# Performance work log

Measured on AMD Instinct MI355X. Metric: run time of the kernel, lower is better.

The kernel has to match this reference:

```python
import jax, jax.numpy as jnp
import numpy as np

N_HEAD = 8

def _l2norm(x, eps=1e-12):
    # F.normalize(p=2, dim=-1): x / max(||x||_2, eps)
    return x / jnp.maximum(jnp.linalg.norm(x, axis=-1, keepdims=True), eps)

def setup_inputs() -> dict:
    key = jax.random.key(0)
    ks = jax.random.split(key, 9)
    B, L, E = 2, 2048, 512
    s = 0.02
    return {
        "query": jax.random.normal(ks[0], (B, L, E), dtype=jnp.float32),
        "Wq": s * jax.random.normal(ks[1], (E, E), dtype=jnp.float32),
        "bq": jnp.zeros((E,), dtype=jnp.float32),
        "Wk": s * jax.random.normal(ks[2], (E, E), dtype=jnp.float32),
        "bk": jnp.zeros((E,), dtype=jnp.float32),
        "Wv": s * jax.random.normal(ks[3], (E, E), dtype=jnp.float32),
        "bv": jnp.zeros((E,), dtype=jnp.float32),
        "Wo": s * jax.random.normal(ks[4], (E, E), dtype=jnp.float32),
        "bo": jnp.zeros((E,), dtype=jnp.float32),
    }

def reference(query, Wq, bq, Wk, bk, Wv, bv, Wo, bo):
    B, L, E = query.shape
    H = N_HEAD
    hd = E // H
    # Faithful to torch: .view(tgt_len, bsz, E) is a RESHAPE, not a transpose.
    x = query.reshape(L, B, E)
    q = jax.nn.relu(x @ Wq.T + bq)
    k = jax.nn.relu(x @ Wk.T + bk)
    v = x @ Wv.T + bv
    q = _l2norm(q)
    k = _l2norm(k)
    # (L, B, E) -> (L, B*H, hd) -> (B*H, L, hd)
    q_ = q.reshape(L, B * H, hd).transpose(1, 0, 2)
    k_ = k.reshape(L, B * H, hd).transpose(1, 0, 2)
    v_ = v.reshape(L, B * H, hd).transpose(1, 0, 2)
    # Causal linear attention: cumulative outer-product of k,v then contract with q.
    kv = jnp.einsum('nld,nlm->nldm', k_, v_)      # [B*H, L, hd, hd]
    kv_cum = jnp.cumsum(kv, axis=1)
    out = jnp.einsum('nld,nldm->nlm', q_, kv_cum)  # [B*H, L, hd]
    out = out.transpose(1, 0, 2).reshape(L, B, E)
    out = out @ Wo.T + bo
    return out.reshape(B, L, E)
```

## Files before the change

kernel.cpp:

```cpp
#include <hip/hip_runtime.h>
#include <hip/hip_bf16.h>

typedef __attribute__((ext_vector_type(8))) short short8;
typedef __attribute__((ext_vector_type(4))) float f32x4;
using bf16 = __hip_bfloat16;

__device__ __forceinline__ unsigned short f2bf(float f) {
    unsigned u = __float_as_uint(f);
    u += 0x7fff + ((u >> 16) & 1);
    return (unsigned short)(u >> 16);
}
__device__ __forceinline__ float bf2f(unsigned short s) {
    return __uint_as_float(((unsigned)s) << 16);
}
__device__ __forceinline__ void gl_lds16(const unsigned short* g, unsigned short* l) {
    __builtin_amdgcn_global_load_lds(
        (const __attribute__((address_space(1))) unsigned int*)g,
        (__attribute__((address_space(3))) unsigned int*)l, 16, 0, 0);
}


__global__ __launch_bounds__(256) void pack_kernel(
    const float* __restrict__ X, const float* __restrict__ Wq, const float* __restrict__ Wk,
    const float* __restrict__ Wv, const float* __restrict__ Wo,
    bf16* __restrict__ Xp, bf16* __restrict__ Wqp, bf16* __restrict__ Wkp,
    bf16* __restrict__ Wvp, bf16* __restrict__ Wop, float* __restrict__ ssq)
{
    __shared__ __align__(16) unsigned short sm[4096];
    int id = blockIdx.x;
    int tid = threadIdx.x;
    if (id < 8) {
        int zi = id * 1024 + tid * 4;
        *(float4*)&ssq[zi] = make_float4(0.f, 0.f, 0.f, 0.f);
    }
    const float* src; unsigned short* dst; int g, sc;
    if (id < 512) { src = X; dst = (unsigned short*)Xp; g = id >> 3; sc = id & 7; }
    else {
        int t = id - 512; int wsel = t >> 6; int u = t & 63;
        g = u >> 3; sc = u & 7;
        src = (wsel == 0) ? Wq : ((wsel == 1) ? Wk : ((wsel == 2) ? Wv : Wo));
        dst = (unsigned short*)((wsel == 0) ? Wqp : ((wsel == 1) ? Wkp : ((wsel == 2) ? Wvp : Wop)));
    }
    int r = tid >> 2, kq = tid & 3;
    const float* sp = src + (size_t)(g * 64 + r) * 512 + sc * 64 + kq * 16;
    #pragma unroll
    for (int i = 0; i < 4; ++i) {
        float4 v = *(const float4*)(sp + i * 4);
        int kk = kq * 16 + i * 4;
        int sl = kk >> 3, el = kk & 7;
        ushort4 u4;
        u4.x = f2bf(v.x); u4.y = f2bf(v.y); u4.z = f2bf(v.z); u4.w = f2bf(v.w);
        *(ushort4*)&sm[(sl * 64 + r) * 8 + el] = u4;
    }
    __syncthreads();
    unsigned short* dp = dst + (size_t)g * 32768 + sc * 4096;
    *(uint4*)(dp + tid * 16)     = *(const uint4*)&sm[tid * 16];
    *(uint4*)(dp + tid * 16 + 8) = *(const uint4*)&sm[tid * 16 + 8];
}

__global__ __launch_bounds__(256) void qkv_gemm_kernel(
    const bf16* __restrict__ Xp,
    const bf16* __restrict__ W0p, const bf16* __restrict__ W1p, const bf16* __restrict__ W2p,
    const float* __restrict__ b0, const float* __restrict__ b1, const float* __restrict__ b2,
    bf16* __restrict__ O0, bf16* __restrict__ O1, bf16* __restrict__ O2,
    float* __restrict__ ssq)
{
    __shared__ __align__(16) unsigned short smem[8192];
    unsigned short* As = smem;
    unsigned short* Bs = smem + 2048;
    int z = blockIdx.z;
    const unsigned short* Wg = (const unsigned short*)((z == 0) ? W0p : ((z == 1) ? W1p : W2p));
    const float* bias = (z == 0) ? b0 : ((z == 1) ? b1 : b2);
    unsigned short* Out = (unsigned short*)((z == 0) ? O0 : ((z == 1) ? O1 : O2));
    const unsigned short* Ag = (const unsigned short*)Xp;

    int g  = blockIdx.x;
    int gB = blockIdx.y * 2;
    int m0 = g * 64;
    int n0 = blockIdx.y * 128;
    int tid = threadIdx.x;
    int lane = tid & 63;
    int w = tid >> 6;
    int wm = (w >> 1) * 32;
    int wn = (w & 1) * 64;
    int fr = lane & 15, qf = lane >> 4;

    f32x4 zero4 = {0.f, 0.f, 0.f, 0.f};
    f32x4 acc[2][4];
    #pragma unroll
    for (int t = 0; t < 2; ++t)
        #pragma unroll
        for (int u = 0; u < 4; ++u) acc[t][u] = zero4;

    for (int kw = 0; kw < 16; ++kw) {
        int s0 = kw * 4;
        __syncthreads();
        gl_lds16(Ag + ((size_t)(g * 64 + s0 + w) * 64 + lane) * 8, As + w * 512);
        gl_lds16(Wg + ((size_t)(gB * 64 + s0 + w) * 64 + lane) * 8, Bs + w * 1024);
        gl_lds16(Wg + ((size_t)((gB + 1) * 64 + s0 + w) * 64 + lane) * 8, Bs + w * 1024 + 512);
        __syncthreads();
        short8 af[2], bfr[4];
        #pragma unroll
        for (int t = 0; t < 2; ++t) af[t] = *(const short8*)&As[(qf * 64 + wm + t * 16 + fr) * 8];
        #pragma unroll
        for (int u = 0; u < 4; ++u) bfr[u] = *(const short8*)&Bs[(qf * 128 + wn + u * 16 + fr) * 8];
        #pragma unroll
        for (int t = 0; t < 2; ++t)
            #pragma unroll
            for (int u = 0; u < 4; ++u)
                acc[t][u] = __builtin_amdgcn_mfma_f32_16x16x32_bf16(af[t], bfr[u], acc[t][u], 0, 0, 0);
    }

    bool relu = (z < 2);
    int rb = qf * 4;
    #pragma unroll
    for (int t = 0; t < 2; ++t)
        #pragma unroll
        for (int u = 0; u < 4; ++u) {
            float bv = bias[n0 + wn + u * 16 + fr];
            #pragma unroll
            for (int r = 0; r < 4; ++r) {
                float v = acc[t][u][r] + bv;
                if (relu) v = fmaxf(v, 0.f);
                acc[t][u][r] = v;
            }
        }
    if (relu) {
        #pragma unroll
        for (int t = 0; t < 2; ++t)
            #pragma unroll
            for (int r = 0; r < 4; ++r) {
                float s = 0.f;
                #pragma unroll
                for (int u = 0; u < 4; ++u) s += acc[t][u][r] * acc[t][u][r];
                #pragma unroll
                for (int off = 1; off < 16; off <<= 1) s += __shfl_xor(s, off, 64);
                if (fr == 0) atomicAdd(&ssq[z * 4096 + m0 + wm + t * 16 + rb + r], s);
            }
    }
    __syncthreads();
    #pragma unroll
    for (int t = 0; t < 2; ++t)
        #pragma unroll
        for (int u = 0; u < 4; ++u)
            #pragma unroll
            for (int r = 0; r < 4; ++r)
                smem[(wm + t * 16 + rb + r) * 128 + wn + u * 16 + fr] = f2bf(acc[t][u][r]);
    __syncthreads();
    #pragma unroll
    for (int rep = 0; rep < 4; ++rep) {
        int idx8 = rep * 256 + tid;
        int row = idx8 >> 4, col8 = (idx8 & 15) * 8;
        *(uint4*)(Out + (size_t)(m0 + row) * 512 + n0 + col8) = *(const uint4*)&smem[row * 128 + col8];
    }
}

__global__ __launch_bounds__(256) void chunk_kv_kernel(
    const bf16* __restrict__ Kb, const bf16* __restrict__ Vb,
    const float* __restrict__ ssq, float* __restrict__ ScT, bf16* __restrict__ Vt_g)
{
    int n = blockIdx.x >> 5, c = blockIdx.x & 31;
    int b = n >> 3, h = n & 7;
    __shared__ float Ks[64 * 64];
    __shared__ float Vs[64 * 64];
    const unsigned short* Kg = (const unsigned short*)Kb;
    const unsigned short* Vg = (const unsigned short*)Vb;
    int tid = threadIdx.x;
    int td = tid >> 4, tm = tid & 15;
    int d0 = td * 4, m0 = tm * 4;
    #pragma unroll
    for (int rep = 0; rep < 4; ++rep) {
        int idx = rep * 1024 + tid * 4;
        int j = idx >> 6, d = idx & 63;
        int grow = (c * 64 + j) * 2 + b;
        ushort4 ku = *(const ushort4*)&Kg[(size_t)grow * 512 + h * 64 + d];
        ushort4 vu = *(const ushort4*)&Vg[(size_t)grow * 512 + h * 64 + d];
        float rk = 1.f / fmaxf(sqrtf(ssq[4096 + grow]), 1e-12f);
        *(float4*)&Ks[j * 64 + d] = make_float4(bf2f(ku.x), bf2f(ku.y), bf2f(ku.z), bf2f(ku.w));
        *(float4*)&Vs[j * 64 + d] = make_float4(bf2f(vu.x) * rk, bf2f(vu.y) * rk,
                                                bf2f(vu.z) * rk, bf2f(vu.w) * rk);
    }
    __syncthreads();
    float acc[4][4] = {};
    for (int j = 0; j < 64; ++j) {
        float4 kv = *(const float4*)&Ks[j * 64 + d0];
        float4 vv = *(const float4*)&Vs[j * 64 + m0];
        acc[0][0] += kv.x*vv.x; acc[0][1] += kv.x*vv.y; acc[0][2] += kv.x*vv.z; acc[0][3] += kv.x*vv.w;
        acc[1][0] += kv.y*vv.x; acc[1][1] += kv.y*vv.y; acc[1][2] += kv.y*vv.z; acc[1][3] += kv.y*vv.w;
        acc[2][0] += kv.z*vv.x; acc[2][1] += kv.z*vv.y; acc[2][2] += kv.z*vv.z; acc[2][3] += kv.z*vv.w;
        acc[3][0] += kv.w*vv.x; acc[3][1] += kv.w*vv.y; acc[3][2] += kv.w*vv.z; acc[3][3] += kv.w*vv.w;
    }
    int vm = tid & 63, vj0 = (tid >> 6) * 16;
    unsigned short tmp[16];
    #pragma unroll
    for (int i = 0; i < 16; ++i) tmp[i] = f2bf(Vs[(vj0 + i) * 64 + vm]);
    size_t vtoff = (size_t)n * 131072 + (size_t)vm * 2048 + c * 64 + vj0;
    *(uint4*)((unsigned short*)Vt_g + vtoff)     = *(uint4*)&tmp[0];
    *(uint4*)((unsigned short*)Vt_g + vtoff + 8) = *(uint4*)&tmp[8];

    float* outp = ScT + (size_t)blockIdx.x * 4096;
    #pragma unroll
    for (int j2 = 0; j2 < 4; ++j2) {
        float4 o4 = make_float4(acc[0][j2], acc[1][j2], acc[2][j2], acc[3][j2]);
        *(float4*)&outp[(m0 + j2) * 64 + d0] = o4;
    }
}

__global__ __launch_bounds__(256) void prefix_kernel(const float* __restrict__ ScT, bf16* __restrict__ SpT)
{
    int n = blockIdx.x >> 4;
    int idx = ((blockIdx.x & 15) << 8) + threadIdx.x;
    size_t base = (size_t)n * 131072 + idx;
    unsigned short* sp = (unsigned short*)SpT;
    float run = 0.f;
    #pragma unroll
    for (int c = 0; c < 32; ++c) {
        size_t off = base + (size_t)c * 4096;
        sp[off] = f2bf(run);
        run += ScT[off];
    }
}

__global__ __launch_bounds__(256) void attn_kernel(
    const bf16* __restrict__ Qb, const bf16* __restrict__ Kb,
    const bf16* __restrict__ Vt_g, const bf16* __restrict__ SpT_g,
    const float* __restrict__ ssq, bf16* __restrict__ AOb)
{
    int n = blockIdx.x >> 5, c = blockIdx.x & 31;
    int b = n >> 3, h = n & 7;
    __shared__ unsigned short Qs[64 * 72];
    __shared__ unsigned short Ks[64 * 72];
    __shared__ unsigned short Vt[64 * 72];
    __shared__ unsigned short Ps[4 * 16 * 40];
    int tid = threadIdx.x;
    int lane = tid & 63;
    int w = tid >> 6;
    int fr = lane & 15, q = lane >> 4;

    const unsigned short* Qg = (const unsigned short*)Qb;
    const unsigned short* Kg = (const unsigned short*)Kb;
    const unsigned short* Vg = (const unsigned short*)Vt_g;

    #pragma unroll
    for (int rep = 0; rep < 2; ++rep) {
        int idx = rep * 256 + tid;
        int l = idx >> 3, dc = (idx & 7) * 8;
        size_t goff = (size_t)((c * 64 + l) * 2 + b) * 512 + h * 64 + dc;
        *(uint4*)&Qs[l * 72 + dc] = *(const uint4*)(Qg + goff);
        *(uint4*)&Ks[l * 72 + dc] = *(const uint4*)(Kg + goff);
        int m = l, jc = dc;
        *(uint4*)&Vt[m * 72 + jc] =
            *(const uint4*)(Vg + (size_t)n * 131072 + (size_t)m * 2048 + c * 64 + jc);
    }
    __syncthreads();

    short8 qf[2];
    #pragma unroll
    for (int kh = 0; kh < 2; ++kh)
        qf[kh] = *(const short8*)&Qs[(w * 16 + fr) * 72 + kh * 32 + q * 8];

    f32x4 zero4 = {0.f, 0.f, 0.f, 0.f};
    f32x4 oacc[4];
    #pragma unroll
    for (int mt = 0; mt < 4; ++mt) oacc[mt] = zero4;

    const unsigned short* spg = (const unsigned short*)SpT_g + (size_t)blockIdx.x * 4096;
    #pragma unroll
    for (int mt = 0; mt < 4; ++mt) {
        #pragma unroll
        for (int kh = 0; kh < 2; ++kh) {
            short8 sf = *(const short8*)&spg[(mt * 16 + fr) * 64 + kh * 32 + q * 8];
            oacc[mt] = __builtin_amdgcn_mfma_f32_16x16x32_bf16(qf[kh], sf, oacc[mt], 0, 0, 0);
        }
    }

    unsigned short* myPs = &Ps[w * 640];
    int rbase = q * 4;
    int njt = (w >> 1) + 1;
    for (int jt = 0; jt < njt; ++jt) {
        f32x4 pacc[2];
        pacc[0] = zero4; pacc[1] = zero4;
        #pragma unroll
        for (int jt16 = 0; jt16 < 2; ++jt16) {
            #pragma unroll
            for (int kh = 0; kh < 2; ++kh) {
                short8 kf = *(const short8*)&Ks[(jt * 32 + jt16 * 16 + fr) * 72 + kh * 32 + q * 8];
                pacc[jt16] = __builtin_amdgcn_mfma_f32_16x16x32_bf16(qf[kh], kf, pacc[jt16], 0, 0, 0);
            }
        }
        bool diag = (jt == njt - 1);
        int lloc = w * 16 + rbase;
        #pragma unroll
        for (int jt16 = 0; jt16 < 2; ++jt16)
            #pragma unroll
            for (int r = 0; r < 4; ++r) {
                int jl = jt * 32 + jt16 * 16 + fr;
                float pv = pacc[jt16][r];
                if (diag && jl > lloc + r) pv = 0.f;
                myPs[(rbase + r) * 40 + jt16 * 16 + fr] = f2bf(pv);
            }
        short8 pf = *(const short8*)&myPs[fr * 40 + q * 8];
        #pragma unroll
        for (int mt = 0; mt < 4; ++mt) {
            short8 vf = *(const short8*)&Vt[(mt * 16 + fr) * 72 + jt * 32 + q * 8];
            oacc[mt] = __builtin_amdgcn_mfma_f32_16x16x32_bf16(pf, vf, oacc[mt], 0, 0, 0);
        }
    }

    float rqv[4];
    #pragma unroll
    for (int r = 0; r < 4; ++r) {
        int flat = (c * 64 + w * 16 + rbase + r) * 2 + b;
        rqv[r] = 1.f / fmaxf(sqrtf(ssq[flat]), 1e-12f);
    }
    __syncthreads();
    #pragma unroll
    for (int mt = 0; mt < 4; ++mt)
        #pragma unroll
        for (int r = 0; r < 4; ++r)
            Qs[(w * 16 + rbase + r) * 64 + mt * 16 + fr] = f2bf(oacc[mt][r] * rqv[r]);
    __syncthreads();
    #pragma unroll
    for (int rep = 0; rep < 2; ++rep) {
        int idx8 = rep * 256 + tid;
        int l = idx8 >> 3, m8 = (idx8 & 7) * 8;
        *(uint4*)((unsigned short*)AOb + (size_t)((c * 64 + l) * 2 + b) * 512 + h * 64 + m8) =
            *(const uint4*)&Qs[l * 64 + m8];
    }
}

__global__ __launch_bounds__(256) void oproj_kernel(
    const bf16* __restrict__ A, const bf16* __restrict__ Wop,
    const float* __restrict__ bias, float* __restrict__ Out)
{
    __shared__ __align__(16) unsigned short smem[8192];
    unsigned short* As = smem;
    unsigned short* Bs = smem + 2560;
    const unsigned short* Ag = (const unsigned short*)A;
    const unsigned short* Wg = (const unsigned short*)Wop;
    int m0 = blockIdx.x * 64;
    int gy = blockIdx.y;
    int n0 = gy * 64;
    int tid = threadIdx.x;
    int lane = tid & 63;
    int w = tid >> 6;
    int fr = lane & 15, qf = lane >> 4;
    int wm = (w >> 1) * 32;
    int wn = (w & 1) * 32;
    int srow = tid >> 2;
    int skk  = (tid & 3) * 8;

    f32x4 zero4 = {0.f, 0.f, 0.f, 0.f};
    f32x4 acc[2][2];
    acc[0][0] = zero4; acc[0][1] = zero4; acc[1][0] = zero4; acc[1][1] = zero4;

    for (int kw = 0; kw < 16; ++kw) {
        int k0 = kw * 32, s0 = kw * 4;
        __syncthreads();
        *(uint4*)&As[srow * 40 + skk] = *(const uint4*)(Ag + (size_t)(m0 + srow) * 512 + k0 + skk);
        gl_lds16(Wg + ((size_t)(gy * 64 + s0 + w) * 64 + lane) * 8, Bs + w * 512);
        __syncthreads();
        short8 af[2], bf[2];
        #pragma unroll
        for (int t = 0; t < 2; ++t) af[t] = *(const short8*)&As[(wm + t * 16 + fr) * 40 + qf * 8];
        #pragma unroll
        for (int u = 0; u < 2; ++u) bf[u] = *(const short8*)&Bs[(qf * 64 + wn + u * 16 + fr) * 8];
        #pragma unroll
        for (int t = 0; t < 2; ++t)
            #pragma unroll
            for (int u = 0; u < 2; ++u)
                acc[t][u] = __builtin_amdgcn_mfma_f32_16x16x32_bf16(af[t], bf[u], acc[t][u], 0, 0, 0);
    }

    int rb = qf * 4;
    float* Cf = (float*)smem;
    __syncthreads();
    #pragma unroll
    for (int t = 0; t < 2; ++t)
        #pragma unroll
        for (int u = 0; u < 2; ++u) {
            float bv = bias[n0 + wn + u * 16 + fr];
            #pragma unroll
            for (int r = 0; r < 4; ++r)
                Cf[(wm + t * 16 + rb + r) * 64 + wn + u * 16 + fr] = acc[t][u][r] + bv;
        }
    __syncthreads();
    #pragma unroll
    for (int rep = 0; rep < 4; ++rep) {
        int idx = rep * 256 + tid;
        int row = idx >> 4, c4 = (idx & 15) * 4;
        *(float4*)(Out + (size_t)(m0 + row) * 512 + n0 + c4) = *(const float4*)&Cf[row * 64 + c4];
    }
}

extern "C" void kernel_launch(void* const* d_in, const int* in_sizes, int n_in,
                              void* d_out, int out_size, void* d_ws, size_t ws_size,
                              hipStream_t stream)
{
    (void)in_sizes; (void)n_in; (void)out_size; (void)ws_size;
    const float* x  = (const float*)d_in[0];
    const float* Wq = (const float*)d_in[1];
    const float* bq = (const float*)d_in[2];
    const float* Wk = (const float*)d_in[3];
    const float* bk = (const float*)d_in[4];
    const float* Wv = (const float*)d_in[5];
    const float* bv = (const float*)d_in[6];
    const float* Wo = (const float*)d_in[7];
    const float* bo = (const float*)d_in[8];
    float* out = (float*)d_out;

    float* ssq = (float*)d_ws;
    bf16* Xp  = (bf16*)(ssq + 8192);
    bf16* Wqp = Xp + 2097152;
    bf16* Wkp = Wqp + 262144;
    bf16* Wvp = Wkp + 262144;
    bf16* Wop = Wvp + 262144;
    bf16* Qb  = Wop + 262144;
    bf16* Kb  = Qb + 2097152;
    bf16* Vb  = Kb + 2097152;
    bf16* Vt  = Vb + 2097152;
    bf16* AOb = Vt + 2097152;
    bf16* SpT = AOb + 2097152;
    float* ScT = (float*)(SpT + 2097152);

    pack_kernel<<<768, 256, 0, stream>>>(x, Wq, Wk, Wv, Wo, Xp, Wqp, Wkp, Wvp, Wop, ssq);
    qkv_gemm_kernel<<<dim3(64, 4, 3), 256, 0, stream>>>(Xp, Wqp, Wkp, Wvp, bq, bk, bv, Qb, Kb, Vb, ssq);
    chunk_kv_kernel<<<dim3(512), 256, 0, stream>>>(Kb, Vb, ssq, ScT, Vt);
    prefix_kernel<<<dim3(256), 256, 0, stream>>>(ScT, SpT);
    attn_kernel<<<dim3(512), 256, 0, stream>>>(Qb, Kb, Vt, SpT, ssq, AOb);
    oproj_kernel<<<dim3(64, 8), 256, 0, stream>>>(AOb, Wop, bo, out);
}
```

Baseline: 121.4 us.

## Double-buffer QKV and output-projection GEMMs; write attention output in packed layout

Both the QKV and output-projection GEMMs now use double-buffered LDS stages with a larger K step per iteration, so global-to-LDS loads for the next stage overlap the MFMAs on the current one and barriers per K are halved. The attention kernel now writes its output in the packed, k-sliced layout that the output projection loads directly with global_load_lds. That removes the strided VGPR-staged A load, and the projection's store remaps rows to match. LDS use per block rises, which may reduce occupancy, and the launch code (not shown) must agree with the new grid mapping.

```diff
diff --git a/kernel.cpp b/kernel.cpp
--- a/kernel.cpp
+++ b/kernel.cpp
@@ -65,9 +65,7 @@
     bf16* __restrict__ O0, bf16* __restrict__ O1, bf16* __restrict__ O2,
     float* __restrict__ ssq)
 {
-    __shared__ __align__(16) unsigned short smem[8192];
-    unsigned short* As = smem;
-    unsigned short* Bs = smem + 2048;
+    __shared__ __align__(16) unsigned short smem[24576];
     int z = blockIdx.z;
     const unsigned short* Wg = (const unsigned short*)((z == 0) ? W0p : ((z == 1) ? W1p : W2p));
     const float* bias = (z == 0) ? b0 : ((z == 1) ? b1 : b2);
@@ -92,24 +90,44 @@
         #pragma unroll
         for (int u = 0; u < 4; ++u) acc[t][u] = zero4;
 
-    for (int kw = 0; kw < 16; ++kw) {
-        int s0 = kw * 4;
+#define QKV_STAGE(buf, it) do {                                                             \
+        unsigned short* As_ = smem + (buf) * 12288;                                         \
+        unsigned short* Bs_ = As_ + 4096;                                                   \
+        int s0_ = (it) * 8;                                                                 \
+        gl_lds16(Ag + ((size_t)(g * 64 + s0_ + w * 2)     * 64 + lane) * 8, As_ + w * 1024);        \
+        gl_lds16(Ag + ((size_t)(g * 64 + s0_ + w * 2 + 1) * 64 + lane) * 8, As_ + w * 1024 + 512);  \
+        gl_lds16(Wg + ((size_t)((gB + (w >> 1)) * 64 + s0_ + (w & 1) * 4)     * 64 + lane) * 8, Bs_ + (w * 4)     * 512); \
+        gl_lds16(Wg + ((size_t)((gB + (w >> 1)) * 64 + s0_ + (w & 1) * 4 + 1) * 64 + lane) * 8, Bs_ + (w * 4 + 1) * 512); \
+        gl_lds16(Wg + ((size_t)((gB + (w >> 1)) * 64 + s0_ + (w & 1) * 4 + 2) * 64 + lane) * 8, Bs_ + (w * 4 + 2) * 512); \
+        gl_lds16(Wg + ((size_t)((gB + (w >> 1)) * 64 + s0_ + (w & 1) * 4 + 3) * 64 + lane) * 8, Bs_ + (w * 4 + 3) * 512); \
+    } while (0)
+
+    int cur = 0;
+    QKV_STAGE(0, 0);
+    __syncthreads();
+    for (int it = 0; it < 8; ++it) {
+        if (it < 7) QKV_STAGE(cur ^ 1, it + 1);
+        const unsigned short* As = smem + cur * 12288;
+        const unsigned short* Bs = As + 4096;
+        #pragma unroll
+        for (int kk = 0; kk < 2; ++kk) {
+            short8 af[2], bfr[4];
+            #pragma unroll
+            for (int t = 0; t < 2; ++t)
+                af[t] = *(const short8*)&As[((kk * 4 + qf) * 64 + wm + t * 16 + fr) * 8];
+            #pragma unroll
+            for (int u = 0; u < 4; ++u)
+                bfr[u] = *(const short8*)&Bs[(((w & 1) * 8 + kk * 4 + qf) * 64 + u * 16 + fr) * 8];
+            #pragma unroll
+            for (int t = 0; t < 2; ++t)
+                #pragma unroll
+                for (int u = 0; u < 4; ++u)
+                    acc[t][u] = __builtin_amdgcn_mfma_f32_16x16x32_bf16(af[t], bfr[u], acc[t][u], 0, 0, 0);
+        }
         __syncthreads();
-        gl_lds16(Ag + ((size_t)(g * 64 + s0 + w) * 64 + lane) * 8, As + w * 512);
-        gl_lds16(Wg + ((size_t)(gB * 64 + s0 + w) * 64 + lane) * 8, Bs + w * 1024);
-        gl_lds16(Wg + ((size_t)((gB + 1) * 64 + s0 + w) * 64 + lane) * 8, Bs + w * 1024 + 512);
-        __syncthreads();
-        short8 af[2], bfr[4];
-        #pragma unroll
-        for (int t = 0; t < 2; ++t) af[t] = *(const short8*)&As[(qf * 64 + wm + t * 16 + fr) * 8];
-        #pragma unroll
-        for (int u = 0; u < 4; ++u) bfr[u] = *(const short8*)&Bs[(qf * 128 + wn + u * 16 + fr) * 8];
-        #pragma unroll
-        for (int t = 0; t < 2; ++t)
-            #pragma unroll
-            for (int u = 0; u < 4; ++u)
-                acc[t][u] = __builtin_amdgcn_mfma_f32_16x16x32_bf16(af[t], bfr[u], acc[t][u], 0, 0, 0);
-    }
+        cur ^= 1;
+    }
+#undef QKV_STAGE
 
     bool relu = (z < 2);
     int rb = qf * 4;
@@ -138,7 +156,6 @@
                 if (fr == 0) atomicAdd(&ssq[z * 4096 + m0 + wm + t * 16 + rb + r], s);
             }
     }
-    __syncthreads();
     #pragma unroll
     for (int t = 0; t < 2; ++t)
         #pragma unroll
@@ -228,10 +245,10 @@
 {
     int n = blockIdx.x >> 5, c = blockIdx.x & 31;
     int b = n >> 3, h = n & 7;
-    __shared__ unsigned short Qs[64 * 72];
-    __shared__ unsigned short Ks[64 * 72];
-    __shared__ unsigned short Vt[64 * 72];
-    __shared__ unsigned short Ps[4 * 16 * 40];
+    __shared__ __align__(16) unsigned short Qs[64 * 72];
+    __shared__ __align__(16) unsigned short Ks[64 * 72];
+    __shared__ __align__(16) unsigned short Vt[64 * 72];
+    __shared__ __align__(16) unsigned short Ps[4 * 16 * 40];
     int tid = threadIdx.x;
     int lane = tid & 63;
     int w = tid >> 6;
@@ -323,9 +340,10 @@
     #pragma unroll
     for (int rep = 0; rep < 2; ++rep) {
         int idx8 = rep * 256 + tid;
-        int l = idx8 >> 3, m8 = (idx8 & 7) * 8;
-        *(uint4*)((unsigned short*)AOb + (size_t)((c * 64 + l) * 2 + b) * 512 + h * 64 + m8) =
-            *(const uint4*)&Qs[l * 64 + m8];
+        int sl = idx8 >> 6, l = idx8 & 63;
+        *(uint4*)((unsigned short*)AOb +
+                  (size_t)(((c * 2 + b) * 64 + h * 8 + sl) * 64 + l) * 8) =
+            *(const uint4*)&Qs[l * 64 + sl * 8];
     }
 }
 
@@ -333,12 +351,10 @@
     const bf16* __restrict__ A, const bf16* __restrict__ Wop,
     const float* __restrict__ bias, float* __restrict__ Out)
 {
-    __shared__ __align__(16) unsigned short smem[8192];
-    unsigned short* As = smem;
-    unsigned short* Bs = smem + 2560;
+    __shared__ __align__(16) unsigned short smem[16384];
     const unsigned short* Ag = (const unsigned short*)A;
     const unsigned short* Wg = (const unsigned short*)Wop;
-    int m0 = blockIdx.x * 64;
+    int gp = blockIdx.x;
     int gy = blockIdx.y;
     int n0 = gy * 64;
     int tid = threadIdx.x;
@@ -347,34 +363,50 @@
     int fr = lane & 15, qf = lane >> 4;
     int wm = (w >> 1) * 32;
     int wn = (w & 1) * 32;
-    int srow = tid >> 2;
-    int skk  = (tid & 3) * 8;
 
     f32x4 zero4 = {0.f, 0.f, 0.f, 0.f};
     f32x4 acc[2][2];
     acc[0][0] = zero4; acc[0][1] = zero4; acc[1][0] = zero4; acc[1][1] = zero4;
 
-    for (int kw = 0; kw < 16; ++kw) {
-        int k0 = kw * 32, s0 = kw * 4;
+#define OPJ_STAGE(buf, it) do {                                                             \
+        unsigned short* As_ = smem + (buf) * 8192;                                          \
+        unsigned short* Bs_ = As_ + 4096;                                                   \
+        int s0_ = (it) * 8;                                                                 \
+        gl_lds16(Ag + ((size_t)(gp * 64 + s0_ + w * 2)     * 64 + lane) * 8, As_ + w * 1024);        \
+        gl_lds16(Ag + ((size_t)(gp * 64 + s0_ + w * 2 + 1) * 64 + lane) * 8, As_ + w * 1024 + 512);  \
+        gl_lds16(Wg + ((size_t)(gy * 64 + s0_ + w * 2)     * 64 + lane) * 8, Bs_ + w * 1024);        \
+        gl_lds16(Wg + ((size_t)(gy * 64 + s0_ + w * 2 + 1) * 64 + lane) * 8, Bs_ + w * 1024 + 512);  \
+    } while (0)
+
+    int cur = 0;
+    OPJ_STAGE(0, 0);
+    __syncthreads();
+    for (int it = 0; it < 8; ++it) {
+        if (it < 7) OPJ_STAGE(cur ^ 1, it + 1);
+        const unsigned short* As = smem + cur * 8192;
+        const unsigned short* Bs = As + 4096;
+        #pragma unroll
+        for (int kk = 0; kk < 2; ++kk) {
+            short8 af[2], bf[2];
+            #pragma unroll
+            for (int t = 0; t < 2; ++t)
+                af[t] = *(const short8*)&As[((kk * 4 + qf) * 64 + wm + t * 16 + fr) * 8];
+            #pragma unroll
+            for (int u = 0; u < 2; ++u)
+                bf[u] = *(const short8*)&Bs[((kk * 4 + qf) * 64 + wn + u * 16 + fr) * 8];
+            #pragma unroll
+            for (int t = 0; t < 2; ++t)
+                #pragma unroll
+                for (int u = 0; u < 2; ++u)
+                    acc[t][u] = __builtin_amdgcn_mfma_f32_16x16x32_bf16(af[t], bf[u], acc[t][u], 0, 0, 0);
+        }
         __syncthreads();
-        *(uint4*)&As[srow * 40 + skk] = *(const uint4*)(Ag + (size_t)(m0 + srow) * 512 + k0 + skk);
-        gl_lds16(Wg + ((size_t)(gy * 64 + s0 + w) * 64 + lane) * 8, Bs + w * 512);
-        __syncthreads();
-        short8 af[2], bf[2];
-        #pragma unroll
-        for (int t = 0; t < 2; ++t) af[t] = *(const short8*)&As[(wm + t * 16 + fr) * 40 + qf * 8];
-        #pragma unroll
-        for (int u = 0; u < 2; ++u) bf[u] = *(const short8*)&Bs[(qf * 64 + wn + u * 16 + fr) * 8];
-        #pragma unroll
-        for (int t = 0; t < 2; ++t)
-            #pragma unroll
-            for (int u = 0; u < 2; ++u)
-                acc[t][u] = __builtin_amdgcn_mfma_f32_16x16x32_bf16(af[t], bf[u], acc[t][u], 0, 0, 0);
-    }
+        cur ^= 1;
+    }
+#undef OPJ_STAGE
 
     int rb = qf * 4;
     float* Cf = (float*)smem;
-    __syncthreads();
     #pragma unroll
     for (int t = 0; t < 2; ++t)
         #pragma unroll
@@ -385,11 +417,12 @@
                 Cf[(wm + t * 16 + rb + r) * 64 + wn + u * 16 + fr] = acc[t][u][r] + bv;
         }
     __syncthreads();
+    int cbase = (gp >> 1) * 128, bb = gp & 1;
     #pragma unroll
     for (int rep = 0; rep < 4; ++rep) {
         int idx = rep * 256 + tid;
-        int row = idx >> 4, c4 = (idx & 15) * 4;
-        *(float4*)(Out + (size_t)(m0 + row) * 512 + n0 + c4) = *(const float4*)&Cf[row * 64 + c4];
+        int l2 = idx >> 4, c4 = (idx & 15) * 4;
+        *(float4*)(Out + (size_t)(cbase + l2 * 2 + bb) * 512 + n0 + c4) = *(const float4*)&Cf[l2 * 64 + c4];
     }
 }
 
```

Result: faster. 116.7 us (-3.9%).
